# Performance work log

Hardware: AMD Instinct MI355X
Metric: run time of the kernel (lower is better)

Reference implementation:

```python
import jax, jax.numpy as jnp
import numpy as np

D_MODEL = 1024
N_HEADS = 16
D_KV = 64
B, S = 2, 2048


def setup_inputs() -> dict:
    key = jax.random.key(0)
    ks = jax.random.split(key, 7)
    scale = 1.0 / np.sqrt(D_MODEL)
    return {
        "query": jax.random.normal(ks[0], (B, S, D_MODEL), jnp.float32),
        "key": jax.random.normal(ks[1], (B, S, D_MODEL), jnp.float32),
        "value": jax.random.normal(ks[2], (B, S, D_MODEL), jnp.float32),
        "mask": jnp.zeros((B, 1, 1, S), jnp.float32),
        "Wq": jax.random.normal(ks[3], (D_MODEL, N_HEADS * D_KV), jnp.float32) * scale,
        "Wk": jax.random.normal(ks[4], (D_MODEL, N_HEADS * D_KV), jnp.float32) * scale,
        "Wv": jax.random.normal(ks[5], (D_MODEL, N_HEADS * D_KV), jnp.float32) * scale,
        "Wo": jax.random.normal(ks[6], (N_HEADS * D_KV, D_MODEL), jnp.float32) * scale,
    }


def _split_heads(x):
    b, s, _ = x.shape
    return x.reshape(b, s, N_HEADS, D_KV).transpose(0, 2, 1, 3)  # [B,H,S,Dk]


def reference(query, key, value, mask, Wq, Wk, Wv, Wo):
    q = _split_heads(query @ Wq)
    k = _split_heads(key @ Wk)
    v = _split_heads(value @ Wv)
    scores = jnp.einsum("bhqd,bhkd->bhqk", q, k) / jnp.sqrt(
        jnp.asarray(D_KV, scores_dtype := q.dtype)
    )
    scores = scores + mask
    attn = jax.nn.softmax(scores, axis=-1)  # dropout_rate=0 -> identity
    ctx = jnp.einsum("bhqk,bhkd->bhqd", attn, v)
    ctx = ctx.transpose(0, 2, 1, 3).reshape(query.shape[0], -1, N_HEADS * D_KV)
    hidden = ctx @ Wo
    return hidden
```

## Files before the change

kernel.cpp:

```cpp
#include <hip/hip_runtime.h>
#include <hip/hip_bf16.h>
#include <stdint.h>

typedef __bf16 bf16;
typedef __bf16 bf16x8 __attribute__((ext_vector_type(8)));
typedef __bf16 bf16x4 __attribute__((ext_vector_type(4)));
typedef float  f32x4  __attribute__((ext_vector_type(4)));

#define S_LEN  2048
#define NH     16
#define DKV    64
#define DMODEL 1024
#define LOG2E  1.4426950408889634f

__device__ __forceinline__ void async_load16(const void* g, void* l) {
  __builtin_amdgcn_global_load_lds(
      (const __attribute__((address_space(1))) uint32_t*)(uintptr_t)g,
      (__attribute__((address_space(3))) uint32_t*)(uintptr_t)l,
      16, 0, 0);
}

__device__ __forceinline__ int sw(int r, int c) {
  return r * 64 + ((((c >> 3) ^ (r & 7)) << 3) | (c & 7));
}

__global__ void cast_qkv(const float* __restrict__ q, const float* __restrict__ k,
                         const float* __restrict__ v,
                         bf16* __restrict__ qo, bf16* __restrict__ ko, bf16* __restrict__ vo)
{
  int z = blockIdx.y;
  const float* in = (z == 0) ? q : (z == 1) ? k : v;
  bf16* out = (z == 0) ? qo : (z == 1) ? ko : vo;
  int i = blockIdx.x * 256 + threadIdx.x;
  const float4* in4 = (const float4*)in;
  float4 a = in4[2 * i];
  float4 c = in4[2 * i + 1];
  bf16x8 o;
  o[0] = (bf16)a.x; o[1] = (bf16)a.y; o[2] = (bf16)a.z; o[3] = (bf16)a.w;
  o[4] = (bf16)c.x; o[5] = (bf16)c.y; o[6] = (bf16)c.z; o[7] = (bf16)c.w;
  ((bf16x8*)out)[i] = o;
}

__global__ void transpose_w(const float* __restrict__ W0, const float* __restrict__ W1,
                            const float* __restrict__ W2, const float* __restrict__ W3,
                            bf16* __restrict__ T0, bf16* __restrict__ T1,
                            bf16* __restrict__ T2, bf16* __restrict__ T3)
{
  int z = blockIdx.z;
  const float* W = (z == 0) ? W0 : (z == 1) ? W1 : (z == 2) ? W2 : W3;
  bf16* T = (z == 0) ? T0 : (z == 1) ? T1 : (z == 2) ? T2 : T3;
  __shared__ float tile[32][33];
  int n0 = blockIdx.x * 32, k0 = blockIdx.y * 32;
  int tx = threadIdx.x, ty = threadIdx.y;
  for (int i = 0; i < 32; i += 8)
    tile[ty + i][tx] = W[(size_t)(k0 + ty + i) * DMODEL + n0 + tx];
  __syncthreads();
  for (int i = 0; i < 32; i += 8)
    T[(size_t)(n0 + ty + i) * DMODEL + k0 + tx] = (bf16)tile[tx][ty + i];
}

template<int TM, int MODE>
__global__ __launch_bounds__(256) void gemm_bt(
    const bf16* __restrict__ A0, const bf16* __restrict__ A1, const bf16* __restrict__ A2,
    const bf16* __restrict__ B0, const bf16* __restrict__ B1, const bf16* __restrict__ B2,
    void* __restrict__ C0, void* __restrict__ C1, void* __restrict__ C2,
    int M, int N, int K)
{
  constexpr int MI = TM / 32;
  __shared__ __align__(16) bf16 As[TM * 32];
  __shared__ __align__(16) bf16 Bs[128 * 32];
  int z = blockIdx.z;
  const bf16* A  = (z == 0) ? A0 : (z == 1) ? A1 : A2;
  const bf16* Bt = (z == 0) ? B0 : (z == 1) ? B1 : B2;
  void* C        = (z == 0) ? C0 : (z == 1) ? C1 : C2;

  const int m0 = blockIdx.y * TM;
  const int n0 = blockIdx.x * 128;
  const int tid = threadIdx.x;
  const int lane = tid & 63;
  const int wave = tid >> 6;
  const int wm = (wave >> 1) * (TM / 2);
  const int wn = (wave & 1) * 64;
  const int row = lane & 15;
  const int quad = lane >> 4;

  f32x4 acc[MI][4];
  for (int i = 0; i < MI; ++i)
    for (int j = 0; j < 4; ++j) acc[i][j] = (f32x4){0.f, 0.f, 0.f, 0.f};

  const int nk = K >> 5;
  for (int kt = 0; kt < nk; ++kt) {
    __syncthreads();
    const int kk = kt << 5;
    for (int j = 0; j < TM / 64; ++j) {
      int base = j * 256 + wave * 64;
      int idx = base + lane;
      int r = idx >> 2;
      int cb = (idx & 3) << 4;
      async_load16((const char*)(A + (size_t)(m0 + r) * K + kk) + cb,
                   (char*)As + (size_t)base * 16);
    }
    for (int j = 0; j < 2; ++j) {
      int base = j * 256 + wave * 64;
      int idx = base + lane;
      int r = idx >> 2;
      int cb = (idx & 3) << 4;
      async_load16((const char*)(Bt + (size_t)(n0 + r) * K + kk) + cb,
                   (char*)Bs + (size_t)base * 16);
    }
    __syncthreads();
    bf16x8 af[MI], bfr[4];
    for (int i = 0; i < MI; ++i)
      af[i] = *(const bf16x8*)(As + (wm + i * 16 + row) * 32 + quad * 8);
    for (int j = 0; j < 4; ++j)
      bfr[j] = *(const bf16x8*)(Bs + (wn + j * 16 + row) * 32 + quad * 8);
    for (int i = 0; i < MI; ++i)
      for (int j = 0; j < 4; ++j)
        acc[i][j] = __builtin_amdgcn_mfma_f32_16x16x32_bf16(af[i], bfr[j], acc[i][j], 0, 0, 0);
  }

  if (MODE == 0) {
    float* Cf = (float*)C;
    for (int i = 0; i < MI; ++i)
      for (int j = 0; j < 4; ++j)
        for (int r = 0; r < 4; ++r) {
          int gm = m0 + wm + i * 16 + quad * 4 + r;
          int gn = n0 + wn + j * 16 + row;
          Cf[(size_t)gm * N + gn] = acc[i][j][r];
        }
  } else if (z != 2) {
    bf16* Cb = (bf16*)C;
    for (int i = 0; i < MI; ++i)
      for (int j = 0; j < 4; ++j)
        for (int r = 0; r < 4; ++r) {
          int gm = m0 + wm + i * 16 + quad * 4 + r;
          int gn = n0 + wn + j * 16 + row;
          int b = gm >> 11, s = gm & 2047;
          int h = gn >> 6,  d = gn & 63;
          Cb[(((size_t)(b * NH + h)) * S_LEN + s) * DKV + d] = (bf16)acc[i][j][r];
        }
  } else {
    bf16* Cb = (bf16*)C;
    for (int i = 0; i < MI; ++i)
      for (int j = 0; j < 4; ++j) {
        int gm = m0 + wm + i * 16 + quad * 4;
        int gn = n0 + wn + j * 16 + row;
        int b = gm >> 11, s = gm & 2047;
        int h = gn >> 6,  d = gn & 63;
        bf16x4 t;
        for (int r = 0; r < 4; ++r) t[r] = (bf16)acc[i][j][r];
        *(bf16x4*)(Cb + (((size_t)(b * NH + h)) * DKV + d) * S_LEN + s) = t;
      }
  }
}

__global__ __launch_bounds__(256, 2) void attn_kernel(
    const bf16* __restrict__ Qh, const bf16* __restrict__ Kh, const bf16* __restrict__ Vth,
    const float* __restrict__ mask, bf16* __restrict__ ctx)
{
  __shared__ __align__(16) bf16 Qs[128 * 64];
  __shared__ __align__(16) bf16 Ks[64 * 64];
  __shared__ __align__(16) bf16 Vts[64 * 64];
  __shared__ __align__(16) bf16 Ps[4][32 * 68];
  __shared__ float masks2[64];

  const int bh = blockIdx.y;
  const int b = bh >> 4;
  const int q0 = blockIdx.x * 128;
  const int tid = threadIdx.x;
  const int lane = tid & 63;
  const int wave = tid >> 6;
  const int row = lane & 15;
  const int quad = lane >> 4;

  {
    int r = tid >> 1;
    int c0 = (tid & 1) * 32;
    const bf16* src = Qh + ((size_t)bh * S_LEN + q0 + r) * DKV + c0;
    for (int u = 0; u < 4; ++u)
      *(bf16x8*)(Qs + sw(r, c0 + u * 8)) = *(const bf16x8*)(src + u * 8);
  }

  float lsum[2][4];
  f32x4 O[2][4];
  for (int i = 0; i < 2; ++i)
    for (int rr = 0; rr < 4; ++rr) lsum[i][rr] = 0.f;
  for (int i = 0; i < 2; ++i)
    for (int j = 0; j < 4; ++j) O[i][j] = (f32x4){0.f, 0.f, 0.f, 0.f};

  const float scale2 = 0.125f * LOG2E;

  for (int kv0 = 0; kv0 < S_LEN; kv0 += 64) {
    __syncthreads();
    {
      int r = tid >> 2;
      int c0 = (tid & 3) * 16;
      const bf16* src = Kh + ((size_t)bh * S_LEN + kv0 + r) * DKV + c0;
      bf16x8 v0 = *(const bf16x8*)src;
      bf16x8 v1 = *(const bf16x8*)(src + 8);
      *(bf16x8*)(Ks + sw(r, c0))     = v0;
      *(bf16x8*)(Ks + sw(r, c0 + 8)) = v1;
    }
    {
      int r = tid >> 2;
      int c0 = (tid & 3) * 16;
      const bf16* src = Vth + ((size_t)bh * DKV + r) * S_LEN + kv0 + c0;
      bf16x8 v0 = *(const bf16x8*)src;
      bf16x8 v1 = *(const bf16x8*)(src + 8);
      *(bf16x8*)(Vts + sw(r, c0))     = v0;
      *(bf16x8*)(Vts + sw(r, c0 + 8)) = v1;
    }
    if (tid < 64) masks2[tid] = mask[b * S_LEN + kv0 + tid] * LOG2E;
    __syncthreads();

    f32x4 sa[2][4];
    for (int i = 0; i < 2; ++i)
      for (int j = 0; j < 4; ++j) sa[i][j] = (f32x4){0.f, 0.f, 0.f, 0.f};
    for (int ks = 0; ks < 2; ++ks) {
      bf16x8 aq[2];
      for (int i = 0; i < 2; ++i)
        aq[i] = *(const bf16x8*)(Qs + sw(wave * 32 + i * 16 + row, ks * 32 + quad * 8));
      for (int j = 0; j < 4; ++j) {
        bf16x8 bk = *(const bf16x8*)(Ks + sw(j * 16 + row, ks * 32 + quad * 8));
        for (int i = 0; i < 2; ++i)
          sa[i][j] = __builtin_amdgcn_mfma_f32_16x16x32_bf16(aq[i], bk, sa[i][j], 0, 0, 0);
      }
    }
    float mk[4];
    for (int j = 0; j < 4; ++j) mk[j] = masks2[j * 16 + row];
    for (int i = 0; i < 2; ++i) {
      bf16* pb = Ps[wave] + (i * 16 + quad * 4) * 68 + row;
      for (int rr = 0; rr < 4; ++rr) {
        float s0 = 0.f;
        for (int j = 0; j < 4; ++j) {
          float p = __builtin_amdgcn_exp2f(sa[i][j][rr] * scale2 + mk[j]);
          s0 += p;
          pb[rr * 68 + j * 16] = (bf16)p;
        }
        lsum[i][rr] += s0;
      }
    }
    __builtin_amdgcn_s_waitcnt(0);

    for (int ks = 0; ks < 2; ++ks) {
      bf16x8 ap[2];
      for (int i = 0; i < 2; ++i) {
        const bf16* pp = Ps[wave] + (i * 16 + row) * 68 + ks * 32 + quad * 8;
        bf16x4 lo = *(const bf16x4*)pp;
        bf16x4 hi = *(const bf16x4*)(pp + 4);
        for (int u = 0; u < 4; ++u) { ap[i][u] = lo[u]; ap[i][u + 4] = hi[u]; }
      }
      for (int j = 0; j < 4; ++j) {
        bf16x8 bv = *(const bf16x8*)(Vts + sw(j * 16 + row, ks * 32 + quad * 8));
        for (int i = 0; i < 2; ++i)
          O[i][j] = __builtin_amdgcn_mfma_f32_16x16x32_bf16(ap[i], bv, O[i][j], 0, 0, 0);
      }
    }
  }

  float rinv[2][4];
  for (int i = 0; i < 2; ++i)
    for (int rr = 0; rr < 4; ++rr) {
      float s0 = lsum[i][rr];
      for (int m = 1; m < 16; m <<= 1) s0 += __shfl_xor(s0, m, 64);
      rinv[i][rr] = 1.f / s0;
    }

  const int h = bh & 15;
  for (int i = 0; i < 2; ++i)
    for (int j = 0; j < 4; ++j)
      for (int rr = 0; rr < 4; ++rr) {
        int gr = q0 + wave * 32 + i * 16 + quad * 4 + rr;
        float v = O[i][j][rr] * rinv[i][rr];
        ctx[((size_t)b * S_LEN + gr) * DMODEL + h * DKV + j * 16 + row] = (bf16)v;
      }
}

extern "C" void kernel_launch(void* const* d_in, const int* in_sizes, int n_in,
                              void* d_out, int out_size, void* d_ws, size_t ws_size,
                              hipStream_t stream)
{
  const float* query = (const float*)d_in[0];
  const float* key_  = (const float*)d_in[1];
  const float* value = (const float*)d_in[2];
  const float* mask  = (const float*)d_in[3];
  const float* Wq = (const float*)d_in[4];
  const float* Wk = (const float*)d_in[5];
  const float* Wv = (const float*)d_in[6];
  const float* Wo = (const float*)d_in[7];

  char* ws = (char*)d_ws;
  const size_t MB = (size_t)1 << 20;
  bf16* qb  = (bf16*)(ws + 0 * MB);
  bf16* kb  = (bf16*)(ws + 8 * MB);
  bf16* vb  = (bf16*)(ws + 16 * MB);
  bf16* wqt = (bf16*)(ws + 24 * MB);
  bf16* wkt = (bf16*)(ws + 26 * MB);
  bf16* wvt = (bf16*)(ws + 28 * MB);
  bf16* wot = (bf16*)(ws + 30 * MB);
  bf16* qh  = (bf16*)(ws + 32 * MB);
  bf16* kh  = (bf16*)(ws + 40 * MB);
  bf16* vth = (bf16*)(ws + 48 * MB);
  bf16* ctx = (bf16*)(ws + 0 * MB);

  cast_qkv<<<dim3(2048, 3), 256, 0, stream>>>(query, key_, value, qb, kb, vb);
  transpose_w<<<dim3(32, 32, 4), dim3(32, 8), 0, stream>>>(Wq, Wk, Wv, Wo, wqt, wkt, wvt, wot);
  gemm_bt<128, 1><<<dim3(8, 32, 3), 256, 0, stream>>>(qb, kb, vb, wqt, wkt, wvt,
                                                      (void*)qh, (void*)kh, (void*)vth,
                                                      4096, 1024, 1024);
  attn_kernel<<<dim3(16, 32), 256, 0, stream>>>(qh, kh, vth, mask, ctx);
  gemm_bt<64, 0><<<dim3(8, 64, 1), 256, 0, stream>>>(ctx, ctx, ctx, wot, wot, wot,
                                                     d_out, d_out, d_out,
                                                     4096, 1024, 1024);
}
```

Baseline: 244.9 us.

## Rewrite attention with 32x32 MFMA, transposed scores kept in registers, mask folded into GEMM

The attention kernel now computes S^T = K·Q^T with 32x32x16 MFMAs, so the exponentiated scores come out already in the A-operand layout for the PV product. This removes the per-wave shared-memory round trip for P. Q is held in registers instead of LDS, and K/V tiles are loaded with asynchronous global-to-LDS copies using an XOR swizzle. The mask is folded into the QK GEMM through an extra K column paired with a constant-1 Q element, and the launch bound is raised to allow more resident blocks. The costs are more register pressure, bf16 rounding of the mask term, and still no overlap of the loads with compute beyond what occupancy provides.

```diff
diff --git a/kernel.cpp b/kernel.cpp
--- a/kernel.cpp
+++ b/kernel.cpp
@@ -6,6 +6,7 @@
 typedef __bf16 bf16x8 __attribute__((ext_vector_type(8)));
 typedef __bf16 bf16x4 __attribute__((ext_vector_type(4)));
 typedef float  f32x4  __attribute__((ext_vector_type(4)));
+typedef float  f32x16 __attribute__((ext_vector_type(16)));
 
 #define S_LEN  2048
 #define NH     16
@@ -18,10 +19,6 @@
       (const __attribute__((address_space(1))) uint32_t*)(uintptr_t)g,
       (__attribute__((address_space(3))) uint32_t*)(uintptr_t)l,
       16, 0, 0);
-}
-
-__device__ __forceinline__ int sw(int r, int c) {
-  return r * 64 + ((((c >> 3) ^ (r & 7)) << 3) | (c & 7));
 }
 
 __global__ void cast_qkv(const float* __restrict__ q, const float* __restrict__ k,
@@ -154,126 +151,116 @@
   }
 }
 
-__global__ __launch_bounds__(256, 2) void attn_kernel(
+__global__ __launch_bounds__(256, 4) void attn_kernel(
     const bf16* __restrict__ Qh, const bf16* __restrict__ Kh, const bf16* __restrict__ Vth,
     const float* __restrict__ mask, bf16* __restrict__ ctx)
 {
-  __shared__ __align__(16) bf16 Qs[128 * 64];
   __shared__ __align__(16) bf16 Ks[64 * 64];
+  __shared__ __align__(16) bf16 Kext[64 * 16];
   __shared__ __align__(16) bf16 Vts[64 * 64];
-  __shared__ __align__(16) bf16 Ps[4][32 * 68];
-  __shared__ float masks2[64];
+  __shared__ __align__(16) float lsumS[4 * 32];
 
   const int bh = blockIdx.y;
   const int b = bh >> 4;
+  const int h = bh & 15;
   const int q0 = blockIdx.x * 128;
   const int tid = threadIdx.x;
   const int lane = tid & 63;
   const int wave = tid >> 6;
-  const int row = lane & 15;
-  const int quad = lane >> 4;
-
+  const int ln = lane & 31;
+  const int hi = lane >> 5;
+  const float SC2 = 0.125f * LOG2E;
+
+  const int qg = q0 + wave * 32 + ln;
+  bf16x8 qf[5];
   {
-    int r = tid >> 1;
-    int c0 = (tid & 1) * 32;
-    const bf16* src = Qh + ((size_t)bh * S_LEN + q0 + r) * DKV + c0;
-    for (int u = 0; u < 4; ++u)
-      *(bf16x8*)(Qs + sw(r, c0 + u * 8)) = *(const bf16x8*)(src + u * 8);
-  }
-
-  float lsum[2][4];
-  f32x4 O[2][4];
-  for (int i = 0; i < 2; ++i)
-    for (int rr = 0; rr < 4; ++rr) lsum[i][rr] = 0.f;
-  for (int i = 0; i < 2; ++i)
-    for (int j = 0; j < 4; ++j) O[i][j] = (f32x4){0.f, 0.f, 0.f, 0.f};
-
-  const float scale2 = 0.125f * LOG2E;
+    const bf16* qrow = Qh + ((size_t)bh * S_LEN + qg) * DKV;
+    for (int c = 0; c < 4; ++c)
+      qf[c] = *(const bf16x8*)(qrow + c * 16 + hi * 8);
+    bf16x8 z;
+    for (int u = 0; u < 8; ++u) z[u] = (bf16)0.f;
+    if (hi == 0) z[0] = (bf16)1.0f;
+    qf[4] = z;
+  }
+
+  f32x16 O[2];
+  for (int nb = 0; nb < 2; ++nb)
+    for (int i = 0; i < 16; ++i) O[nb][i] = 0.f;
+  float lsum = 0.f;
 
   for (int kv0 = 0; kv0 < S_LEN; kv0 += 64) {
     __syncthreads();
-    {
-      int r = tid >> 2;
-      int c0 = (tid & 3) * 16;
-      const bf16* src = Kh + ((size_t)bh * S_LEN + kv0 + r) * DKV + c0;
-      bf16x8 v0 = *(const bf16x8*)src;
-      bf16x8 v1 = *(const bf16x8*)(src + 8);
-      *(bf16x8*)(Ks + sw(r, c0))     = v0;
-      *(bf16x8*)(Ks + sw(r, c0 + 8)) = v1;
-    }
-    {
-      int r = tid >> 2;
-      int c0 = (tid & 3) * 16;
-      const bf16* src = Vth + ((size_t)bh * DKV + r) * S_LEN + kv0 + c0;
-      bf16x8 v0 = *(const bf16x8*)src;
-      bf16x8 v1 = *(const bf16x8*)(src + 8);
-      *(bf16x8*)(Vts + sw(r, c0))     = v0;
-      *(bf16x8*)(Vts + sw(r, c0 + 8)) = v1;
-    }
-    if (tid < 64) masks2[tid] = mask[b * S_LEN + kv0 + tid] * LOG2E;
+    for (int j = 0; j < 2; ++j) {
+      int base = j * 256 + wave * 64;
+      int idx = base + lane;
+      int r = idx >> 3;
+      int cc = (idx & 7) ^ (r & 7);
+      async_load16(Kh + ((size_t)bh * S_LEN + kv0 + r) * DKV + cc * 8,
+                   (char*)Ks + (size_t)base * 16);
+      async_load16(Vth + ((size_t)bh * DKV + r) * S_LEN + kv0 + cc * 8,
+                   (char*)Vts + (size_t)base * 16);
+    }
+    if (tid < 64) {
+      float m8 = mask[b * S_LEN + kv0 + tid] * 8.0f;
+      bf16x8 e0, zz;
+      for (int u = 0; u < 8; ++u) { e0[u] = (bf16)0.f; zz[u] = (bf16)0.f; }
+      e0[0] = (bf16)m8;
+      *(bf16x8*)(Kext + tid * 16)     = e0;
+      *(bf16x8*)(Kext + tid * 16 + 8) = zz;
+    }
     __syncthreads();
 
-    f32x4 sa[2][4];
-    for (int i = 0; i < 2; ++i)
-      for (int j = 0; j < 4; ++j) sa[i][j] = (f32x4){0.f, 0.f, 0.f, 0.f};
-    for (int ks = 0; ks < 2; ++ks) {
-      bf16x8 aq[2];
-      for (int i = 0; i < 2; ++i)
-        aq[i] = *(const bf16x8*)(Qs + sw(wave * 32 + i * 16 + row, ks * 32 + quad * 8));
+    f32x16 Sm[2];
+    for (int i = 0; i < 16; ++i) { Sm[0][i] = 0.f; Sm[1][i] = 0.f; }
+    for (int c = 0; c < 5; ++c) {
+      bf16x8 k0, k1;
+      if (c < 4) {
+        k0 = *(const bf16x8*)(Ks + (ln)      * 64 + (((2 * c + hi) ^ (ln & 7)) << 3));
+        k1 = *(const bf16x8*)(Ks + (32 + ln) * 64 + (((2 * c + hi) ^ (ln & 7)) << 3));
+      } else {
+        k0 = *(const bf16x8*)(Kext + ln * 16 + hi * 8);
+        k1 = *(const bf16x8*)(Kext + (32 + ln) * 16 + hi * 8);
+      }
+      Sm[0] = __builtin_amdgcn_mfma_f32_32x32x16_bf16(k0, qf[c], Sm[0], 0, 0, 0);
+      Sm[1] = __builtin_amdgcn_mfma_f32_32x32x16_bf16(k1, qf[c], Sm[1], 0, 0, 0);
+    }
+
+    for (int cg = 0; cg < 4; ++cg) {
+      int mb = cg >> 1, g = cg & 1;
+      bf16x8 ap;
+      float ls0 = 0.f;
+      for (int u = 0; u < 8; ++u) {
+        float p = __builtin_amdgcn_exp2f(Sm[mb][g * 8 + u] * SC2);
+        ls0 += p;
+        ap[u] = (bf16)p;
+      }
+      lsum += ls0;
+      for (int nb = 0; nb < 2; ++nb) {
+        int d = nb * 32 + ln;
+        int ch0 = ((2 * g + 4 * mb))     ^ (d & 7);
+        int ch1 = ((1 + 2 * g + 4 * mb)) ^ (d & 7);
+        bf16x4 lo = *(const bf16x4*)(Vts + d * 64 + ch0 * 8 + hi * 4);
+        bf16x4 hv = *(const bf16x4*)(Vts + d * 64 + ch1 * 8 + hi * 4);
+        bf16x8 bv;
+        for (int u = 0; u < 4; ++u) { bv[u] = lo[u]; bv[u + 4] = hv[u]; }
+        O[nb] = __builtin_amdgcn_mfma_f32_32x32x16_bf16(ap, bv, O[nb], 0, 0, 0);
+      }
+    }
+  }
+
+  float lt = lsum + __shfl_xor(lsum, 32, 64);
+  if (lane < 32) lsumS[wave * 32 + lane] = 1.0f / lt;
+  __builtin_amdgcn_s_waitcnt(0);
+
+  for (int g = 0; g < 4; ++g) {
+    f32x4 ri = *(const f32x4*)(lsumS + wave * 32 + g * 8 + hi * 4);
+    for (int nb = 0; nb < 2; ++nb)
       for (int j = 0; j < 4; ++j) {
-        bf16x8 bk = *(const bf16x8*)(Ks + sw(j * 16 + row, ks * 32 + quad * 8));
-        for (int i = 0; i < 2; ++i)
-          sa[i][j] = __builtin_amdgcn_mfma_f32_16x16x32_bf16(aq[i], bk, sa[i][j], 0, 0, 0);
-      }
-    }
-    float mk[4];
-    for (int j = 0; j < 4; ++j) mk[j] = masks2[j * 16 + row];
-    for (int i = 0; i < 2; ++i) {
-      bf16* pb = Ps[wave] + (i * 16 + quad * 4) * 68 + row;
-      for (int rr = 0; rr < 4; ++rr) {
-        float s0 = 0.f;
-        for (int j = 0; j < 4; ++j) {
-          float p = __builtin_amdgcn_exp2f(sa[i][j][rr] * scale2 + mk[j]);
-          s0 += p;
-          pb[rr * 68 + j * 16] = (bf16)p;
-        }
-        lsum[i][rr] += s0;
-      }
-    }
-    __builtin_amdgcn_s_waitcnt(0);
-
-    for (int ks = 0; ks < 2; ++ks) {
-      bf16x8 ap[2];
-      for (int i = 0; i < 2; ++i) {
-        const bf16* pp = Ps[wave] + (i * 16 + row) * 68 + ks * 32 + quad * 8;
-        bf16x4 lo = *(const bf16x4*)pp;
-        bf16x4 hi = *(const bf16x4*)(pp + 4);
-        for (int u = 0; u < 4; ++u) { ap[i][u] = lo[u]; ap[i][u + 4] = hi[u]; }
-      }
-      for (int j = 0; j < 4; ++j) {
-        bf16x8 bv = *(const bf16x8*)(Vts + sw(j * 16 + row, ks * 32 + quad * 8));
-        for (int i = 0; i < 2; ++i)
-          O[i][j] = __builtin_amdgcn_mfma_f32_16x16x32_bf16(ap[i], bv, O[i][j], 0, 0, 0);
-      }
-    }
-  }
-
-  float rinv[2][4];
-  for (int i = 0; i < 2; ++i)
-    for (int rr = 0; rr < 4; ++rr) {
-      float s0 = lsum[i][rr];
-      for (int m = 1; m < 16; m <<= 1) s0 += __shfl_xor(s0, m, 64);
-      rinv[i][rr] = 1.f / s0;
-    }
-
-  const int h = bh & 15;
-  for (int i = 0; i < 2; ++i)
-    for (int j = 0; j < 4; ++j)
-      for (int rr = 0; rr < 4; ++rr) {
-        int gr = q0 + wave * 32 + i * 16 + quad * 4 + rr;
-        float v = O[i][j][rr] * rinv[i][rr];
-        ctx[((size_t)b * S_LEN + gr) * DMODEL + h * DKV + j * 16 + row] = (bf16)v;
-      }
+        int qrow = q0 + wave * 32 + j + 8 * g + 4 * hi;
+        float v = O[nb][g * 4 + j] * ri[j];
+        ctx[((size_t)b * S_LEN + qrow) * DMODEL + h * DKV + nb * 32 + ln] = (bf16)v;
+      }
+  }
 }
 
 extern "C" void kernel_launch(void* const* d_in, const int* in_sizes, int n_in,
```

Measured after the change: 251.5 us. 1.03x slower.
